# Kernel tuning notes

Hardware: AMD Instinct MI355X
Metric: run time of the kernel (lower is better)

The kernel has to match this reference:

```python
import jax, jax.numpy as jnp
import numpy as np

N_USER = 250_000
N_ITEM = 250_000
E = 500_000
IN, H, C = 128, 64, 2
NEG_SLOPE = 0.01  # torch F.leaky_relu default


def setup_inputs() -> dict:
    key = jax.random.key(0)
    ks = jax.random.split(key, 24)
    d = {}
    d["feat_user"] = jax.random.normal(ks[0], (N_USER, IN), jnp.float32)
    d["feat_item"] = jax.random.normal(ks[1], (N_ITEM, IN), jnp.float32)
    # per-etype linear params, layer 1 (in_feats -> h_dim)
    s1 = 1.0 / np.sqrt(IN)
    d["W1_follows"] = jax.random.normal(ks[2], (IN, H), jnp.float32) * s1
    d["b1_follows"] = jax.random.normal(ks[3], (H,), jnp.float32) * s1
    d["W1_clicks"]  = jax.random.normal(ks[4], (IN, H), jnp.float32) * s1
    d["b1_clicks"]  = jax.random.normal(ks[5], (H,), jnp.float32) * s1
    d["W1_rev"]     = jax.random.normal(ks[6], (IN, H), jnp.float32) * s1
    d["b1_rev"]     = jax.random.normal(ks[7], (H,), jnp.float32) * s1
    # per-etype linear params, layer 2 (h_dim -> num_classes)
    s2 = 1.0 / np.sqrt(H)
    d["W2_follows"] = jax.random.normal(ks[8], (H, C), jnp.float32) * s2
    d["b2_follows"] = jax.random.normal(ks[9], (C,), jnp.float32) * s2
    d["W2_clicks"]  = jax.random.normal(ks[10], (H, C), jnp.float32) * s2
    d["b2_clicks"]  = jax.random.normal(ks[11], (C,), jnp.float32) * s2
    d["W2_rev"]     = jax.random.normal(ks[12], (H, C), jnp.float32) * s2
    d["b2_rev"]     = jax.random.normal(ks[13], (C,), jnp.float32) * s2
    # edge lists: (src, dst) per canonical etype
    d["follows_src"] = jax.random.randint(ks[14], (E,), 0, N_USER, jnp.int32)  # user->user
    d["follows_dst"] = jax.random.randint(ks[15], (E,), 0, N_USER, jnp.int32)
    d["clicks_src"]  = jax.random.randint(ks[16], (E,), 0, N_USER, jnp.int32)  # user->item
    d["clicks_dst"]  = jax.random.randint(ks[17], (E,), 0, N_ITEM, jnp.int32)
    d["rev_src"]     = jax.random.randint(ks[18], (E,), 0, N_ITEM, jnp.int32)  # item->user
    d["rev_dst"]     = jax.random.randint(ks[19], (E,), 0, N_USER, jnp.int32)
    return d


def _mean_agg(Wh, src, dst, n_dst):
    # copy_u + mean: gather transformed src feats per edge, segment-mean onto dst
    m = Wh[src]                                                   # [E, d]
    s = jax.ops.segment_sum(m, dst, num_segments=n_dst)           # [n_dst, d]
    deg = jax.ops.segment_sum(jnp.ones_like(dst, Wh.dtype), dst, num_segments=n_dst)
    return s / jnp.maximum(deg, 1.0)[:, None]                     # 0 for deg-0 nodes (DGL fills 0)


def _layer(fu, fi, Wf, bf, Wc, bc, Wr, br,
           fsrc, fdst, csrc, cdst, rsrc, rdst):
    # per-etype linear on src features, per-etype mean, cross-etype 'sum'
    h_user = (_mean_agg(fu @ Wf + bf, fsrc, fdst, N_USER)
              + _mean_agg(fi @ Wr + br, rsrc, rdst, N_USER))
    h_item = _mean_agg(fu @ Wc + bc, csrc, cdst, N_ITEM)
    return h_user, h_item


def reference(feat_user, feat_item,
              W1_follows, b1_follows, W1_clicks, b1_clicks, W1_rev, b1_rev,
              W2_follows, b2_follows, W2_clicks, b2_clicks, W2_rev, b2_rev,
              follows_src, follows_dst, clicks_src, clicks_dst, rev_src, rev_dst):
    h1u, h1i = _layer(feat_user, feat_item,
                      W1_follows, b1_follows, W1_clicks, b1_clicks, W1_rev, b1_rev,
                      follows_src, follows_dst, clicks_src, clicks_dst, rev_src, rev_dst)
    h2u = jnp.where(h1u >= 0, h1u, NEG_SLOPE * h1u)
    h2i = jnp.where(h1i >= 0, h1i, NEG_SLOPE * h1i)
    out_u, out_i = _layer(h2u, h2i,
                          W2_follows, b2_follows, W2_clicks, b2_clicks, W2_rev, b2_rev,
                          follows_src, follows_dst, clicks_src, clicks_dst, rev_src, rev_dst)
    # (h_dict, h_dict_2) flattened per ntype
    return (out_u, out_i, h2u, h2i)
```

## Files before the change

### kernel.cpp

```cpp
#include <hip/hip_runtime.h>
#include <cstdio>

#define NU 250000
#define NI 250000
#define NE 500000
#define ND 250000
#define NB_SCAN 245
#define NR 8
#define RSZ 31250

typedef __attribute__((ext_vector_type(8))) short short8v;
typedef __attribute__((ext_vector_type(4))) float float4v;

__device__ inline unsigned short f2bf(float x) {
  unsigned int b = __float_as_uint(x);
  unsigned int r = (b + 0x7FFFu + ((b >> 16) & 1u)) >> 16;
  return (unsigned short)r;
}
__device__ inline float bf2f(unsigned short u) {
  return __uint_as_float(((unsigned int)u) << 16);
}

__device__ inline void async_copy16(const float* g, float* l) {
  __builtin_amdgcn_global_load_lds((const __attribute__((address_space(1))) void*)g,
                                   (__attribute__((address_space(3))) void*)l, 16, 0, 0);
}

__global__ void hist3_kernel(const int* __restrict__ fdst, const int* __restrict__ cdst,
                             const int* __restrict__ rdst,
                             int* __restrict__ degf, int* __restrict__ degc, int* __restrict__ degr) {
  int i = blockIdx.x * blockDim.x + threadIdx.x;
  if (i < NE) {
    atomicAdd(&degf[fdst[i]], 1);
    atomicAdd(&degc[cdst[i]], 1);
    atomicAdd(&degr[rdst[i]], 1);
  }
}

__global__ void scan1_kernel(const int* __restrict__ deg0, const int* __restrict__ deg1,
                             const int* __restrict__ deg2, int* __restrict__ bsum) {
  const int* deg = blockIdx.y == 0 ? deg0 : (blockIdx.y == 1 ? deg1 : deg2);
  int* bs = bsum + blockIdx.y * 256;
  __shared__ int s[256];
  int b = blockIdx.x, t = threadIdx.x;
  int base = b * 1024 + t * 4;
  int v = 0;
  #pragma unroll
  for (int i = 0; i < 4; ++i) if (base + i < ND) v += deg[base + i];
  s[t] = v; __syncthreads();
  for (int off = 128; off > 0; off >>= 1) { if (t < off) s[t] += s[t + off]; __syncthreads(); }
  if (t == 0) bs[b] = s[0];
}

__global__ void scan2_kernel(int* __restrict__ bsum) {
  int* bs = bsum + blockIdx.x * 256;
  __shared__ int s[256];
  int t = threadIdx.x;
  s[t] = (t < NB_SCAN) ? bs[t] : 0;
  __syncthreads();
  for (int off = 1; off < 256; off <<= 1) {
    int x = (t >= off) ? s[t - off] : 0;
    __syncthreads();
    s[t] += x;
    __syncthreads();
  }
  if (t < NB_SCAN) bs[t] = (t == 0) ? 0 : s[t - 1];
}

__global__ void scan3_kernel(const int* __restrict__ deg0, const int* __restrict__ deg1,
                             const int* __restrict__ deg2, const int* __restrict__ bsum,
                             int* __restrict__ offs0, int* __restrict__ offs1, int* __restrict__ offs2,
                             int* __restrict__ cur0, int* __restrict__ cur1, int* __restrict__ cur2) {
  int y = blockIdx.y;
  const int* deg = y == 0 ? deg0 : (y == 1 ? deg1 : deg2);
  int* offs = y == 0 ? offs0 : (y == 1 ? offs1 : offs2);
  int* cursor = y == 0 ? cur0 : (y == 1 ? cur1 : cur2);
  const int* bs = bsum + y * 256;
  __shared__ int s[256];
  int b = blockIdx.x, t = threadIdx.x;
  int base = b * 1024 + t * 4;
  int v[4]; int sum = 0;
  #pragma unroll
  for (int i = 0; i < 4; ++i) { v[i] = (base + i < ND) ? deg[base + i] : 0; sum += v[i]; }
  s[t] = sum; __syncthreads();
  for (int off = 1; off < 256; off <<= 1) {
    int x = (t >= off) ? s[t - off] : 0;
    __syncthreads();
    s[t] += x;
    __syncthreads();
  }
  int run = bs[b] + s[t] - sum;
  #pragma unroll
  for (int i = 0; i < 4; ++i) {
    if (base + i < ND) { offs[base + i] = run; cursor[base + i] = run; run += v[i]; }
  }
  if (b == 0 && t == 0) offs[ND] = NE;
}

__global__ void bucket_part_kernel(const int* __restrict__ fsrc, const int* __restrict__ fdst,
                                   const int* __restrict__ csrc, const int* __restrict__ cdst,
                                   const int* __restrict__ rsrc, const int* __restrict__ rdst,
                                   int* __restrict__ curf, int* __restrict__ curc, int* __restrict__ curr,
                                   int* __restrict__ srtf, int* __restrict__ srtc, int* __restrict__ srtr) {
  const int r = blockIdx.x & (NR - 1);
  const int chunk = blockIdx.x >> 3;
  const int lo = r * RSZ, hi = lo + RSZ;
  const int base = chunk * 1024;
  #pragma unroll
  for (int i = 0; i < 4; ++i) {
    int e = base + i * 256 + threadIdx.x;
    if (e < NE) {
      int d0 = fdst[e]; int s0 = fsrc[e];
      if (d0 >= lo && d0 < hi) { int p = atomicAdd(&curf[d0], 1); srtf[p] = s0; }
      int d1 = cdst[e]; int s1 = csrc[e];
      if (d1 >= lo && d1 < hi) { int p = atomicAdd(&curc[d1], 1); srtc[p] = s1; }
      int d2 = rdst[e]; int s2 = rsrc[e];
      if (d2 >= lo && d2 < hi) { int p = atomicAdd(&curr[d2], 1); srtr[p] = s2; }
    }
  }
}

__global__ void prepw_kernel(const float* __restrict__ W0, const float* __restrict__ W1,
                             const float* __restrict__ W2, unsigned short* __restrict__ T) {
  int gt = blockIdx.x * 256 + threadIdx.x;
  int et = gt >> 10;
  int g = gt & 1023;
  int gl = g & 63;
  int jm = (g >> 6) & 3;
  int c = g >> 8;
  int kb = c * 32 + (gl >> 4) * 8;
  int col = jm * 16 + (gl & 15);
  const float* W = et == 0 ? W0 : (et == 1 ? W1 : W2);
  short8v u;
  #pragma unroll
  for (int i = 0; i < 8; ++i) u[i] = (short)f2bf(W[(kb + i) * 64 + col]);
  ((short8v*)T)[gt] = u;
}

template <bool TWO>
__global__ __launch_bounds__(256, 2) void gemm_dma_kernel(
    const float* __restrict__ X, int n, int ntiles,
    const unsigned short* __restrict__ Ta, const float* __restrict__ ba,
    const unsigned short* __restrict__ Tb, const float* __restrict__ bb,
    unsigned short* __restrict__ Ya, unsigned short* __restrict__ Yb) {
  __shared__ float sx[2][64 * 128];
  const int tid = threadIdx.x;
  const int lane = tid & 63;
  const int wave = tid >> 6;
  const int cb = (lane >> 4) * 4;

  short8v A[4][4], B[4][4];
  #pragma unroll
  for (int c = 0; c < 4; ++c) {
    #pragma unroll
    for (int jm = 0; jm < 4; ++jm) {
      A[c][jm] = ((const short8v*)Ta)[c * 256 + jm * 64 + lane];
      if constexpr (TWO) B[c][jm] = ((const short8v*)Tb)[c * 256 + jm * 64 + lane];
    }
  }
  float4 bias_a[4], bias_b[4];
  #pragma unroll
  for (int jm = 0; jm < 4; ++jm) {
    bias_a[jm] = *(const float4*)&ba[jm * 16 + cb];
    if constexpr (TWO) bias_b[jm] = *(const float4*)&bb[jm * 16 + cb];
  }

  const int nl = wave * 16 + (lane & 15);
  const int sw = nl & 7;

  int t = blockIdx.x;
  {
    #pragma unroll
    for (int j = 0; j < 8; ++j) {
      int idx = (wave * 8 + j) * 64 + lane;
      int row = idx >> 5, u = idx & 31;
      int gr = t * 64 + row; if (gr >= n) gr = n - 1;
      const float* src = X + (size_t)gr * 128 + ((u ^ (row & 7)) << 2);
      float* dst = &sx[0][(wave * 8 + j) * 256];
      async_copy16(src, dst);
    }
  }
  asm volatile("s_waitcnt vmcnt(0)" ::: "memory");
  __syncthreads();

  int cur = 0;
  while (true) {
    int tn = t + (int)gridDim.x;
    bool more = (tn < ntiles);
    if (more) {
      #pragma unroll
      for (int j = 0; j < 8; ++j) {
        int idx = (wave * 8 + j) * 64 + lane;
        int row = idx >> 5, u = idx & 31;
        int gr = tn * 64 + row; if (gr >= n) gr = n - 1;
        const float* src = X + (size_t)gr * 128 + ((u ^ (row & 7)) << 2);
        float* dst = &sx[cur ^ 1][(wave * 8 + j) * 256];
        async_copy16(src, dst);
      }
    }

    float4v accA[4] = {};
    float4v accB[4] = {};
    #pragma unroll
    for (int c = 0; c < 4; ++c) {
      int s0 = c * 8 + (lane >> 4) * 2;
      float4 f0 = *(const float4*)&sx[cur][nl * 128 + (((s0 + 0) ^ sw) << 2)];
      float4 f1 = *(const float4*)&sx[cur][nl * 128 + (((s0 + 1) ^ sw) << 2)];
      short8v bfr;
      bfr[0] = (short)f2bf(f0.x); bfr[1] = (short)f2bf(f0.y);
      bfr[2] = (short)f2bf(f0.z); bfr[3] = (short)f2bf(f0.w);
      bfr[4] = (short)f2bf(f1.x); bfr[5] = (short)f2bf(f1.y);
      bfr[6] = (short)f2bf(f1.z); bfr[7] = (short)f2bf(f1.w);
      #pragma unroll
      for (int jm = 0; jm < 4; ++jm) {
        accA[jm] = __builtin_amdgcn_mfma_f32_16x16x32_bf16(A[c][jm], bfr, accA[jm], 0, 0, 0);
        if constexpr (TWO)
          accB[jm] = __builtin_amdgcn_mfma_f32_16x16x32_bf16(B[c][jm], bfr, accB[jm], 0, 0, 0);
      }
    }
    int node = t * 64 + nl;
    if (node < n) {
      #pragma unroll
      for (int jm = 0; jm < 4; ++jm) {
        ushort4 o;
        o.x = f2bf(accA[jm][0] + bias_a[jm].x);
        o.y = f2bf(accA[jm][1] + bias_a[jm].y);
        o.z = f2bf(accA[jm][2] + bias_a[jm].z);
        o.w = f2bf(accA[jm][3] + bias_a[jm].w);
        *(ushort4*)&Ya[(size_t)node * 64 + jm * 16 + cb] = o;
        if constexpr (TWO) {
          ushort4 o2;
          o2.x = f2bf(accB[jm][0] + bias_b[jm].x);
          o2.y = f2bf(accB[jm][1] + bias_b[jm].y);
          o2.z = f2bf(accB[jm][2] + bias_b[jm].z);
          o2.w = f2bf(accB[jm][3] + bias_b[jm].w);
          *(ushort4*)&Yb[(size_t)node * 64 + jm * 16 + cb] = o2;
        }
      }
    }

    if (!more) break;
    asm volatile("s_waitcnt vmcnt(0)" ::: "memory");
    __syncthreads();
    cur ^= 1;
    t = tn;
  }
}

__global__ __launch_bounds__(256) void agg_user_kernel(
    const unsigned short* __restrict__ Whf, const unsigned short* __restrict__ Whr,
    const int* __restrict__ offs_f, const int* __restrict__ srt_f,
    const int* __restrict__ offs_r, const int* __restrict__ srt_r,
    const float* __restrict__ W2f, const float* __restrict__ b2f,
    const float* __restrict__ W2c, const float* __restrict__ b2c,
    float* __restrict__ h2u, float* __restrict__ Y2f, float* __restrict__ Y2c) {
  int t = blockIdx.x * 256 + threadIdx.x;
  int d = t >> 4, q = t & 15;
  if (d >= NU) return;

  float af[4] = {0.f, 0.f, 0.f, 0.f};
  int f0 = offs_f[d], f1 = offs_f[d + 1];
  for (int e = f0; e < f1; ++e) {
    int s = srt_f[e];
    ushort4 v = *(const ushort4*)&Whf[(size_t)s * 64 + q * 4];
    af[0] += bf2f(v.x); af[1] += bf2f(v.y); af[2] += bf2f(v.z); af[3] += bf2f(v.w);
  }
  float rf = 1.0f / fmaxf((float)(f1 - f0), 1.0f);

  float ar[4] = {0.f, 0.f, 0.f, 0.f};
  int r0 = offs_r[d], r1 = offs_r[d + 1];
  for (int e = r0; e < r1; ++e) {
    int s = srt_r[e];
    ushort4 v = *(const ushort4*)&Whr[(size_t)s * 64 + q * 4];
    ar[0] += bf2f(v.x); ar[1] += bf2f(v.y); ar[2] += bf2f(v.z); ar[3] += bf2f(v.w);
  }
  float rr = 1.0f / fmaxf((float)(r1 - r0), 1.0f);

  float h[4];
  #pragma unroll
  for (int i = 0; i < 4; ++i) {
    float x = af[i] * rf + ar[i] * rr;
    h[i] = x >= 0.f ? x : 0.01f * x;
  }
  *(float4*)&h2u[(size_t)d * 64 + q * 4] = make_float4(h[0], h[1], h[2], h[3]);

  float pf0 = 0.f, pf1 = 0.f, pc0 = 0.f, pc1 = 0.f;
  #pragma unroll
  for (int i = 0; i < 4; ++i) {
    int j = q * 4 + i;
    pf0 += h[i] * W2f[j * 2 + 0]; pf1 += h[i] * W2f[j * 2 + 1];
    pc0 += h[i] * W2c[j * 2 + 0]; pc1 += h[i] * W2c[j * 2 + 1];
  }
  #pragma unroll
  for (int off = 1; off < 16; off <<= 1) {
    pf0 += __shfl_xor(pf0, off, 64);
    pf1 += __shfl_xor(pf1, off, 64);
    pc0 += __shfl_xor(pc0, off, 64);
    pc1 += __shfl_xor(pc1, off, 64);
  }
  if (q == 0) {
    Y2f[(size_t)d * 2 + 0] = pf0 + b2f[0];
    Y2f[(size_t)d * 2 + 1] = pf1 + b2f[1];
    Y2c[(size_t)d * 2 + 0] = pc0 + b2c[0];
    Y2c[(size_t)d * 2 + 1] = pc1 + b2c[1];
  }
}

__global__ __launch_bounds__(256) void agg_item_kernel(
    const unsigned short* __restrict__ Whc,
    const int* __restrict__ offs_c, const int* __restrict__ srt_c,
    const float* __restrict__ W2r, const float* __restrict__ b2r,
    float* __restrict__ h2i, float* __restrict__ Y2r) {
  int t = blockIdx.x * 256 + threadIdx.x;
  int d = t >> 4, q = t & 15;
  if (d >= NI) return;

  float ac[4] = {0.f, 0.f, 0.f, 0.f};
  int c0 = offs_c[d], c1 = offs_c[d + 1];
  for (int e = c0; e < c1; ++e) {
    int s = srt_c[e];
    ushort4 v = *(const ushort4*)&Whc[(size_t)s * 64 + q * 4];
    ac[0] += bf2f(v.x); ac[1] += bf2f(v.y); ac[2] += bf2f(v.z); ac[3] += bf2f(v.w);
  }
  float rc = 1.0f / fmaxf((float)(c1 - c0), 1.0f);

  float h[4];
  #pragma unroll
  for (int i = 0; i < 4; ++i) {
    float x = ac[i] * rc;
    h[i] = x >= 0.f ? x : 0.01f * x;
  }
  *(float4*)&h2i[(size_t)d * 64 + q * 4] = make_float4(h[0], h[1], h[2], h[3]);

  float p0 = 0.f, p1 = 0.f;
  #pragma unroll
  for (int i = 0; i < 4; ++i) {
    int j = q * 4 + i;
    p0 += h[i] * W2r[j * 2 + 0]; p1 += h[i] * W2r[j * 2 + 1];
  }
  #pragma unroll
  for (int off = 1; off < 16; off <<= 1) {
    p0 += __shfl_xor(p0, off, 64);
    p1 += __shfl_xor(p1, off, 64);
  }
  if (q == 0) {
    Y2r[(size_t)d * 2 + 0] = p0 + b2r[0];
    Y2r[(size_t)d * 2 + 1] = p1 + b2r[1];
  }
}

__global__ void out_user_kernel(const float* __restrict__ Y2f, const float* __restrict__ Y2r,
                                const int* __restrict__ offs_f, const int* __restrict__ srt_f,
                                const int* __restrict__ offs_r, const int* __restrict__ srt_r,
                                float* __restrict__ out_u) {
  int d = blockIdx.x * blockDim.x + threadIdx.x;
  if (d >= NU) return;
  int f0 = offs_f[d], f1 = offs_f[d + 1];
  float a0 = 0.f, a1 = 0.f;
  for (int e = f0; e < f1; ++e) {
    int s = srt_f[e];
    a0 += Y2f[(size_t)s * 2 + 0]; a1 += Y2f[(size_t)s * 2 + 1];
  }
  float rf = 1.0f / fmaxf((float)(f1 - f0), 1.0f);
  int r0 = offs_r[d], r1 = offs_r[d + 1];
  float c0 = 0.f, c1 = 0.f;
  for (int e = r0; e < r1; ++e) {
    int s = srt_r[e];
    c0 += Y2r[(size_t)s * 2 + 0]; c1 += Y2r[(size_t)s * 2 + 1];
  }
  float rr = 1.0f / fmaxf((float)(r1 - r0), 1.0f);
  out_u[(size_t)d * 2 + 0] = a0 * rf + c0 * rr;
  out_u[(size_t)d * 2 + 1] = a1 * rf + c1 * rr;
}

__global__ void out_item_kernel(const float* __restrict__ Y2c,
                                const int* __restrict__ offs_c, const int* __restrict__ srt_c,
                                float* __restrict__ out_i) {
  int d = blockIdx.x * blockDim.x + threadIdx.x;
  if (d >= NI) return;
  int c0o = offs_c[d], c1o = offs_c[d + 1];
  float a0 = 0.f, a1 = 0.f;
  for (int e = c0o; e < c1o; ++e) {
    int s = srt_c[e];
    a0 += Y2c[(size_t)s * 2 + 0]; a1 += Y2c[(size_t)s * 2 + 1];
  }
  float rc = 1.0f / fmaxf((float)(c1o - c0o), 1.0f);
  out_i[(size_t)d * 2 + 0] = a0 * rc;
  out_i[(size_t)d * 2 + 1] = a1 * rc;
}

extern "C" void kernel_launch(void* const* d_in, const int* in_sizes, int n_in,
                              void* d_out, int out_size, void* d_ws, size_t ws_size,
                              hipStream_t stream) {
  const float* feat_user = (const float*)d_in[0];
  const float* feat_item = (const float*)d_in[1];
  const float* W1f = (const float*)d_in[2];  const float* b1f = (const float*)d_in[3];
  const float* W1c = (const float*)d_in[4];  const float* b1c = (const float*)d_in[5];
  const float* W1r = (const float*)d_in[6];  const float* b1r = (const float*)d_in[7];
  const float* W2f = (const float*)d_in[8];  const float* b2f = (const float*)d_in[9];
  const float* W2c = (const float*)d_in[10]; const float* b2c = (const float*)d_in[11];
  const float* W2r = (const float*)d_in[12]; const float* b2r = (const float*)d_in[13];
  const int* fsrc = (const int*)d_in[14];  const int* fdst = (const int*)d_in[15];
  const int* csrc = (const int*)d_in[16];  const int* cdst = (const int*)d_in[17];
  const int* rsrc = (const int*)d_in[18];  const int* rdst = (const int*)d_in[19];

  float* out = (float*)d_out;
  float* out_u = out;
  float* out_i = out + 2 * NU;
  float* h2u  = out + 1000000;
  float* h2i  = out + 17000000;

  unsigned short* Whf = (unsigned short*)d_ws;
  unsigned short* Whc = Whf + 16000000;
  unsigned short* Whr = Whc + 16000000;
  unsigned short* Wtab = Whr + 16000000;
  unsigned short* Tf = Wtab;
  unsigned short* Tc = Wtab + 8192;
  unsigned short* Tr = Wtab + 16384;
  int* ibase = (int*)(Wtab + 24576);
  const int P = 250304;
  int* offs_f = ibase;            int* offs_c = offs_f + P;  int* offs_r = offs_c + P;
  int* cur_f  = offs_r + P;       int* cur_c  = cur_f + P;   int* cur_r  = cur_c + P;
  int* deg_f  = cur_r + P;        int* deg_c  = deg_f + P;   int* deg_r  = deg_c + P;
  int* srt_f  = deg_r + P;
  int* srt_c  = srt_f + 500096;
  int* srt_r  = srt_c + 500096;
  int* bsum   = srt_r + 500096;
  float* Y2f  = (float*)(bsum + 768);
  float* Y2c  = Y2f + 500000;
  float* Y2r  = Y2c + 500000;

  size_t need = 96000000ull + 24576ull * 2ull
              + (9ull * P + 3ull * 500096ull + 768ull + 1500000ull) * 4ull;
  if (ws_size < need) {
    fprintf(stderr, "kernel_launch: ws too small (%zu < %zu)\n", ws_size, need);
    return;
  }

  hipMemsetAsync(deg_f, 0, (size_t)(3 * P) * 4, stream);

  const int eb = (NE + 255) / 256;

  prepw_kernel<<<12, 256, 0, stream>>>(W1f, W1c, W1r, Wtab);

  const int utiles = (NU + 63) / 64;
  const int itiles = (NI + 63) / 64;
  gemm_dma_kernel<true><<<512, 256, 0, stream>>>(feat_user, NU, utiles, Tf, b1f, Tc, b1c, Whf, Whc);
  gemm_dma_kernel<false><<<512, 256, 0, stream>>>(feat_item, NI, itiles, Tr, b1r, nullptr, nullptr, Whr, nullptr);

  hist3_kernel<<<eb, 256, 0, stream>>>(fdst, cdst, rdst, deg_f, deg_c, deg_r);
  scan1_kernel<<<dim3(NB_SCAN, 3), 256, 0, stream>>>(deg_f, deg_c, deg_r, bsum);
  scan2_kernel<<<3, 256, 0, stream>>>(bsum);
  scan3_kernel<<<dim3(NB_SCAN, 3), 256, 0, stream>>>(deg_f, deg_c, deg_r, bsum,
                                                     offs_f, offs_c, offs_r,
                                                     cur_f, cur_c, cur_r);
  const int chunks = (NE + 1023) / 1024;
  bucket_part_kernel<<<chunks * NR, 256, 0, stream>>>(fsrc, fdst, csrc, cdst, rsrc, rdst,
                                                      cur_f, cur_c, cur_r, srt_f, srt_c, srt_r);

  const int ab = (NU * 16 + 255) / 256;
  agg_user_kernel<<<ab, 256, 0, stream>>>(Whf, Whr, offs_f, srt_f, offs_r, srt_r,
                                          W2f, b2f, W2c, b2c, h2u, Y2f, Y2c);
  agg_item_kernel<<<ab, 256, 0, stream>>>(Whc, offs_c, srt_c, W2r, b2r, h2i, Y2r);

  const int nb = (NU + 255) / 256;
  out_user_kernel<<<nb, 256, 0, stream>>>(Y2f, Y2r, offs_f, srt_f, offs_r, srt_r, out_u);
  out_item_kernel<<<nb, 256, 0, stream>>>(Y2c, offs_c, srt_c, out_i);
}
```

Before: 353.6 us.

## Fuse user/item aggregation kernels and interleave gathers for memory-level parallelism

Merges the user and item aggregation kernels into one launch, and the two output kernels into another, using a block-index split. Each 16-lane group now handles two destination nodes, and the follows and rev edge lists are walked together in one loop, so several independent gathers are in flight per iteration. The aim is more overlap of gather latency and fewer launches. In exchange the code is more divergent and uses more registers, and there are fewer threads per node.

```diff
diff --git a/kernel.cpp b/kernel.cpp
--- a/kernel.cpp
+++ b/kernel.cpp
@@ -247,146 +247,177 @@
   }
 }
 
-__global__ __launch_bounds__(256) void agg_user_kernel(
+__global__ __launch_bounds__(256) void agg_fused_kernel(
     const unsigned short* __restrict__ Whf, const unsigned short* __restrict__ Whr,
+    const unsigned short* __restrict__ Whc,
     const int* __restrict__ offs_f, const int* __restrict__ srt_f,
     const int* __restrict__ offs_r, const int* __restrict__ srt_r,
+    const int* __restrict__ offs_c, const int* __restrict__ srt_c,
     const float* __restrict__ W2f, const float* __restrict__ b2f,
     const float* __restrict__ W2c, const float* __restrict__ b2c,
-    float* __restrict__ h2u, float* __restrict__ Y2f, float* __restrict__ Y2c) {
-  int t = blockIdx.x * 256 + threadIdx.x;
-  int d = t >> 4, q = t & 15;
-  if (d >= NU) return;
-
-  float af[4] = {0.f, 0.f, 0.f, 0.f};
-  int f0 = offs_f[d], f1 = offs_f[d + 1];
-  for (int e = f0; e < f1; ++e) {
-    int s = srt_f[e];
-    ushort4 v = *(const ushort4*)&Whf[(size_t)s * 64 + q * 4];
-    af[0] += bf2f(v.x); af[1] += bf2f(v.y); af[2] += bf2f(v.z); af[3] += bf2f(v.w);
-  }
-  float rf = 1.0f / fmaxf((float)(f1 - f0), 1.0f);
-
-  float ar[4] = {0.f, 0.f, 0.f, 0.f};
-  int r0 = offs_r[d], r1 = offs_r[d + 1];
-  for (int e = r0; e < r1; ++e) {
-    int s = srt_r[e];
-    ushort4 v = *(const ushort4*)&Whr[(size_t)s * 64 + q * 4];
-    ar[0] += bf2f(v.x); ar[1] += bf2f(v.y); ar[2] += bf2f(v.z); ar[3] += bf2f(v.w);
-  }
-  float rr = 1.0f / fmaxf((float)(r1 - r0), 1.0f);
-
-  float h[4];
-  #pragma unroll
-  for (int i = 0; i < 4; ++i) {
-    float x = af[i] * rf + ar[i] * rr;
-    h[i] = x >= 0.f ? x : 0.01f * x;
-  }
-  *(float4*)&h2u[(size_t)d * 64 + q * 4] = make_float4(h[0], h[1], h[2], h[3]);
-
-  float pf0 = 0.f, pf1 = 0.f, pc0 = 0.f, pc1 = 0.f;
-  #pragma unroll
-  for (int i = 0; i < 4; ++i) {
-    int j = q * 4 + i;
-    pf0 += h[i] * W2f[j * 2 + 0]; pf1 += h[i] * W2f[j * 2 + 1];
-    pc0 += h[i] * W2c[j * 2 + 0]; pc1 += h[i] * W2c[j * 2 + 1];
-  }
-  #pragma unroll
-  for (int off = 1; off < 16; off <<= 1) {
-    pf0 += __shfl_xor(pf0, off, 64);
-    pf1 += __shfl_xor(pf1, off, 64);
-    pc0 += __shfl_xor(pc0, off, 64);
-    pc1 += __shfl_xor(pc1, off, 64);
-  }
-  if (q == 0) {
-    Y2f[(size_t)d * 2 + 0] = pf0 + b2f[0];
-    Y2f[(size_t)d * 2 + 1] = pf1 + b2f[1];
-    Y2c[(size_t)d * 2 + 0] = pc0 + b2c[0];
-    Y2c[(size_t)d * 2 + 1] = pc1 + b2c[1];
-  }
-}
-
-__global__ __launch_bounds__(256) void agg_item_kernel(
-    const unsigned short* __restrict__ Whc,
-    const int* __restrict__ offs_c, const int* __restrict__ srt_c,
     const float* __restrict__ W2r, const float* __restrict__ b2r,
-    float* __restrict__ h2i, float* __restrict__ Y2r) {
-  int t = blockIdx.x * 256 + threadIdx.x;
-  int d = t >> 4, q = t & 15;
-  if (d >= NI) return;
-
-  float ac[4] = {0.f, 0.f, 0.f, 0.f};
-  int c0 = offs_c[d], c1 = offs_c[d + 1];
-  for (int e = c0; e < c1; ++e) {
-    int s = srt_c[e];
-    ushort4 v = *(const ushort4*)&Whc[(size_t)s * 64 + q * 4];
-    ac[0] += bf2f(v.x); ac[1] += bf2f(v.y); ac[2] += bf2f(v.z); ac[3] += bf2f(v.w);
-  }
-  float rc = 1.0f / fmaxf((float)(c1 - c0), 1.0f);
-
-  float h[4];
-  #pragma unroll
-  for (int i = 0; i < 4; ++i) {
-    float x = ac[i] * rc;
-    h[i] = x >= 0.f ? x : 0.01f * x;
-  }
-  *(float4*)&h2i[(size_t)d * 64 + q * 4] = make_float4(h[0], h[1], h[2], h[3]);
-
-  float p0 = 0.f, p1 = 0.f;
-  #pragma unroll
-  for (int i = 0; i < 4; ++i) {
-    int j = q * 4 + i;
-    p0 += h[i] * W2r[j * 2 + 0]; p1 += h[i] * W2r[j * 2 + 1];
-  }
-  #pragma unroll
-  for (int off = 1; off < 16; off <<= 1) {
-    p0 += __shfl_xor(p0, off, 64);
-    p1 += __shfl_xor(p1, off, 64);
-  }
-  if (q == 0) {
-    Y2r[(size_t)d * 2 + 0] = p0 + b2r[0];
-    Y2r[(size_t)d * 2 + 1] = p1 + b2r[1];
-  }
-}
-
-__global__ void out_user_kernel(const float* __restrict__ Y2f, const float* __restrict__ Y2r,
-                                const int* __restrict__ offs_f, const int* __restrict__ srt_f,
-                                const int* __restrict__ offs_r, const int* __restrict__ srt_r,
-                                float* __restrict__ out_u) {
-  int d = blockIdx.x * blockDim.x + threadIdx.x;
-  if (d >= NU) return;
-  int f0 = offs_f[d], f1 = offs_f[d + 1];
-  float a0 = 0.f, a1 = 0.f;
-  for (int e = f0; e < f1; ++e) {
-    int s = srt_f[e];
-    a0 += Y2f[(size_t)s * 2 + 0]; a1 += Y2f[(size_t)s * 2 + 1];
-  }
-  float rf = 1.0f / fmaxf((float)(f1 - f0), 1.0f);
-  int r0 = offs_r[d], r1 = offs_r[d + 1];
-  float c0 = 0.f, c1 = 0.f;
-  for (int e = r0; e < r1; ++e) {
-    int s = srt_r[e];
-    c0 += Y2r[(size_t)s * 2 + 0]; c1 += Y2r[(size_t)s * 2 + 1];
-  }
-  float rr = 1.0f / fmaxf((float)(r1 - r0), 1.0f);
-  out_u[(size_t)d * 2 + 0] = a0 * rf + c0 * rr;
-  out_u[(size_t)d * 2 + 1] = a1 * rf + c1 * rr;
-}
-
-__global__ void out_item_kernel(const float* __restrict__ Y2c,
-                                const int* __restrict__ offs_c, const int* __restrict__ srt_c,
-                                float* __restrict__ out_i) {
-  int d = blockIdx.x * blockDim.x + threadIdx.x;
-  if (d >= NI) return;
-  int c0o = offs_c[d], c1o = offs_c[d + 1];
-  float a0 = 0.f, a1 = 0.f;
-  for (int e = c0o; e < c1o; ++e) {
-    int s = srt_c[e];
-    a0 += Y2c[(size_t)s * 2 + 0]; a1 += Y2c[(size_t)s * 2 + 1];
-  }
-  float rc = 1.0f / fmaxf((float)(c1o - c0o), 1.0f);
-  out_i[(size_t)d * 2 + 0] = a0 * rc;
-  out_i[(size_t)d * 2 + 1] = a1 * rc;
+    float* __restrict__ h2u, float* __restrict__ h2i,
+    float* __restrict__ Y2f, float* __restrict__ Y2c, float* __restrict__ Y2r,
+    int ub) {
+  const int tid = threadIdx.x;
+  const int gid = tid >> 4;
+  const int q = tid & 15;
+
+  if (blockIdx.x < ub) {
+    int d0 = (blockIdx.x * 16 + gid) * 2;
+    int d1 = d0 + 1;
+    bool v0 = d0 < NU, v1 = d1 < NU;
+    int ef0 = v0 ? offs_f[d0] : 0, ef0e = v0 ? offs_f[d0 + 1] : 0;
+    int ef1 = v1 ? offs_f[d1] : 0, ef1e = v1 ? offs_f[d1 + 1] : 0;
+    int er0 = v0 ? offs_r[d0] : 0, er0e = v0 ? offs_r[d0 + 1] : 0;
+    int er1 = v1 ? offs_r[d1] : 0, er1e = v1 ? offs_r[d1 + 1] : 0;
+    float rf0 = 1.0f / fmaxf((float)(ef0e - ef0), 1.0f);
+    float rf1 = 1.0f / fmaxf((float)(ef1e - ef1), 1.0f);
+    float rr0 = 1.0f / fmaxf((float)(er0e - er0), 1.0f);
+    float rr1 = 1.0f / fmaxf((float)(er1e - er1), 1.0f);
+
+    float af0[4] = {0, 0, 0, 0}, af1[4] = {0, 0, 0, 0};
+    float ar0[4] = {0, 0, 0, 0}, ar1[4] = {0, 0, 0, 0};
+    while (ef0 < ef0e || ef1 < ef1e || er0 < er0e || er1 < er1e) {
+      bool hf0 = ef0 < ef0e, hf1 = ef1 < ef1e, hr0 = er0 < er0e, hr1 = er1 < er1e;
+      ushort4 vf0, vf1, vr0, vr1;
+      if (hf0) { int s = srt_f[ef0]; vf0 = *(const ushort4*)&Whf[(size_t)s * 64 + q * 4]; }
+      if (hf1) { int s = srt_f[ef1]; vf1 = *(const ushort4*)&Whf[(size_t)s * 64 + q * 4]; }
+      if (hr0) { int s = srt_r[er0]; vr0 = *(const ushort4*)&Whr[(size_t)s * 64 + q * 4]; }
+      if (hr1) { int s = srt_r[er1]; vr1 = *(const ushort4*)&Whr[(size_t)s * 64 + q * 4]; }
+      if (hf0) { af0[0] += bf2f(vf0.x); af0[1] += bf2f(vf0.y); af0[2] += bf2f(vf0.z); af0[3] += bf2f(vf0.w); ++ef0; }
+      if (hf1) { af1[0] += bf2f(vf1.x); af1[1] += bf2f(vf1.y); af1[2] += bf2f(vf1.z); af1[3] += bf2f(vf1.w); ++ef1; }
+      if (hr0) { ar0[0] += bf2f(vr0.x); ar0[1] += bf2f(vr0.y); ar0[2] += bf2f(vr0.z); ar0[3] += bf2f(vr0.w); ++er0; }
+      if (hr1) { ar1[0] += bf2f(vr1.x); ar1[1] += bf2f(vr1.y); ar1[2] += bf2f(vr1.z); ar1[3] += bf2f(vr1.w); ++er1; }
+    }
+
+    float h0v[4], h1v[4];
+    #pragma unroll
+    for (int i = 0; i < 4; ++i) {
+      float x0 = af0[i] * rf0 + ar0[i] * rr0;
+      h0v[i] = x0 >= 0.f ? x0 : 0.01f * x0;
+      float x1 = af1[i] * rf1 + ar1[i] * rr1;
+      h1v[i] = x1 >= 0.f ? x1 : 0.01f * x1;
+    }
+    if (v0) *(float4*)&h2u[(size_t)d0 * 64 + q * 4] = make_float4(h0v[0], h0v[1], h0v[2], h0v[3]);
+    if (v1) *(float4*)&h2u[(size_t)d1 * 64 + q * 4] = make_float4(h1v[0], h1v[1], h1v[2], h1v[3]);
+
+    float pf00 = 0, pf01 = 0, pc00 = 0, pc01 = 0;
+    float pf10 = 0, pf11 = 0, pc10 = 0, pc11 = 0;
+    #pragma unroll
+    for (int i = 0; i < 4; ++i) {
+      int j = q * 4 + i;
+      float wf0 = W2f[j * 2 + 0], wf1 = W2f[j * 2 + 1];
+      float wc0 = W2c[j * 2 + 0], wc1 = W2c[j * 2 + 1];
+      pf00 += h0v[i] * wf0; pf01 += h0v[i] * wf1;
+      pc00 += h0v[i] * wc0; pc01 += h0v[i] * wc1;
+      pf10 += h1v[i] * wf0; pf11 += h1v[i] * wf1;
+      pc10 += h1v[i] * wc0; pc11 += h1v[i] * wc1;
+    }
+    #pragma unroll
+    for (int off = 1; off < 16; off <<= 1) {
+      pf00 += __shfl_xor(pf00, off, 64); pf01 += __shfl_xor(pf01, off, 64);
+      pc00 += __shfl_xor(pc00, off, 64); pc01 += __shfl_xor(pc01, off, 64);
+      pf10 += __shfl_xor(pf10, off, 64); pf11 += __shfl_xor(pf11, off, 64);
+      pc10 += __shfl_xor(pc10, off, 64); pc11 += __shfl_xor(pc11, off, 64);
+    }
+    if (q == 0) {
+      if (v0) {
+        Y2f[(size_t)d0 * 2 + 0] = pf00 + b2f[0]; Y2f[(size_t)d0 * 2 + 1] = pf01 + b2f[1];
+        Y2c[(size_t)d0 * 2 + 0] = pc00 + b2c[0]; Y2c[(size_t)d0 * 2 + 1] = pc01 + b2c[1];
+      }
+      if (v1) {
+        Y2f[(size_t)d1 * 2 + 0] = pf10 + b2f[0]; Y2f[(size_t)d1 * 2 + 1] = pf11 + b2f[1];
+        Y2c[(size_t)d1 * 2 + 0] = pc10 + b2c[0]; Y2c[(size_t)d1 * 2 + 1] = pc11 + b2c[1];
+      }
+    }
+  } else {
+    int d0 = ((blockIdx.x - ub) * 16 + gid) * 2;
+    int d1 = d0 + 1;
+    bool v0 = d0 < NI, v1 = d1 < NI;
+    int ec0 = v0 ? offs_c[d0] : 0, ec0e = v0 ? offs_c[d0 + 1] : 0;
+    int ec1 = v1 ? offs_c[d1] : 0, ec1e = v1 ? offs_c[d1 + 1] : 0;
+    float rc0 = 1.0f / fmaxf((float)(ec0e - ec0), 1.0f);
+    float rc1 = 1.0f / fmaxf((float)(ec1e - ec1), 1.0f);
+
+    float ac0[4] = {0, 0, 0, 0}, ac1[4] = {0, 0, 0, 0};
+    while (ec0 < ec0e || ec1 < ec1e) {
+      bool h0 = ec0 < ec0e, h1 = ec1 < ec1e;
+      ushort4 v0v, v1v;
+      if (h0) { int s = srt_c[ec0]; v0v = *(const ushort4*)&Whc[(size_t)s * 64 + q * 4]; }
+      if (h1) { int s = srt_c[ec1]; v1v = *(const ushort4*)&Whc[(size_t)s * 64 + q * 4]; }
+      if (h0) { ac0[0] += bf2f(v0v.x); ac0[1] += bf2f(v0v.y); ac0[2] += bf2f(v0v.z); ac0[3] += bf2f(v0v.w); ++ec0; }
+      if (h1) { ac1[0] += bf2f(v1v.x); ac1[1] += bf2f(v1v.y); ac1[2] += bf2f(v1v.z); ac1[3] += bf2f(v1v.w); ++ec1; }
+    }
+
+    float h0v[4], h1v[4];
+    #pragma unroll
+    for (int i = 0; i < 4; ++i) {
+      float x0 = ac0[i] * rc0;
+      h0v[i] = x0 >= 0.f ? x0 : 0.01f * x0;
+      float x1 = ac1[i] * rc1;
+      h1v[i] = x1 >= 0.f ? x1 : 0.01f * x1;
+    }
+    if (v0) *(float4*)&h2i[(size_t)d0 * 64 + q * 4] = make_float4(h0v[0], h0v[1], h0v[2], h0v[3]);
+    if (v1) *(float4*)&h2i[(size_t)d1 * 64 + q * 4] = make_float4(h1v[0], h1v[1], h1v[2], h1v[3]);
+
+    float p00 = 0, p01 = 0, p10 = 0, p11 = 0;
+    #pragma unroll
+    for (int i = 0; i < 4; ++i) {
+      int j = q * 4 + i;
+      float w0 = W2r[j * 2 + 0], w1 = W2r[j * 2 + 1];
+      p00 += h0v[i] * w0; p01 += h0v[i] * w1;
+      p10 += h1v[i] * w0; p11 += h1v[i] * w1;
+    }
+    #pragma unroll
+    for (int off = 1; off < 16; off <<= 1) {
+      p00 += __shfl_xor(p00, off, 64); p01 += __shfl_xor(p01, off, 64);
+      p10 += __shfl_xor(p10, off, 64); p11 += __shfl_xor(p11, off, 64);
+    }
+    if (q == 0) {
+      if (v0) { Y2r[(size_t)d0 * 2 + 0] = p00 + b2r[0]; Y2r[(size_t)d0 * 2 + 1] = p01 + b2r[1]; }
+      if (v1) { Y2r[(size_t)d1 * 2 + 0] = p10 + b2r[0]; Y2r[(size_t)d1 * 2 + 1] = p11 + b2r[1]; }
+    }
+  }
+}
+
+__global__ void out_fused_kernel(const float* __restrict__ Y2f, const float* __restrict__ Y2r,
+                                 const float* __restrict__ Y2c,
+                                 const int* __restrict__ offs_f, const int* __restrict__ srt_f,
+                                 const int* __restrict__ offs_r, const int* __restrict__ srt_r,
+                                 const int* __restrict__ offs_c, const int* __restrict__ srt_c,
+                                 float* __restrict__ out_u, float* __restrict__ out_i, int ub) {
+  if (blockIdx.x < ub) {
+    int d = blockIdx.x * 256 + threadIdx.x;
+    if (d >= NU) return;
+    int f = offs_f[d], f1 = offs_f[d + 1];
+    int r = offs_r[d], r1 = offs_r[d + 1];
+    float rf = 1.0f / fmaxf((float)(f1 - f), 1.0f);
+    float rr = 1.0f / fmaxf((float)(r1 - r), 1.0f);
+    float a0 = 0.f, a1 = 0.f, c0 = 0.f, c1 = 0.f;
+    while (f < f1 || r < r1) {
+      bool hf = f < f1, hr = r < r1;
+      float2 yf, yr;
+      if (hf) { int s = srt_f[f]; yf = *(const float2*)&Y2f[(size_t)s * 2]; }
+      if (hr) { int s = srt_r[r]; yr = *(const float2*)&Y2r[(size_t)s * 2]; }
+      if (hf) { a0 += yf.x; a1 += yf.y; ++f; }
+      if (hr) { c0 += yr.x; c1 += yr.y; ++r; }
+    }
+    out_u[(size_t)d * 2 + 0] = a0 * rf + c0 * rr;
+    out_u[(size_t)d * 2 + 1] = a1 * rf + c1 * rr;
+  } else {
+    int d = (blockIdx.x - ub) * 256 + threadIdx.x;
+    if (d >= NI) return;
+    int c = offs_c[d], c1e = offs_c[d + 1];
+    float rc = 1.0f / fmaxf((float)(c1e - c), 1.0f);
+    float a0 = 0.f, a1 = 0.f;
+    for (; c < c1e; ++c) {
+      int s = srt_c[c];
+      a0 += Y2c[(size_t)s * 2 + 0]; a1 += Y2c[(size_t)s * 2 + 1];
+    }
+    out_i[(size_t)d * 2 + 0] = a0 * rc;
+    out_i[(size_t)d * 2 + 1] = a1 * rc;
+  }
 }
 
 extern "C" void kernel_launch(void* const* d_in, const int* in_sizes, int n_in,
@@ -458,12 +489,14 @@
   bucket_part_kernel<<<chunks * NR, 256, 0, stream>>>(fsrc, fdst, csrc, cdst, rsrc, rdst,
                                                       cur_f, cur_c, cur_r, srt_f, srt_c, srt_r);
 
-  const int ab = (NU * 16 + 255) / 256;
-  agg_user_kernel<<<ab, 256, 0, stream>>>(Whf, Whr, offs_f, srt_f, offs_r, srt_r,
-                                          W2f, b2f, W2c, b2c, h2u, Y2f, Y2c);
-  agg_item_kernel<<<ab, 256, 0, stream>>>(Whc, offs_c, srt_c, W2r, b2r, h2i, Y2r);
-
-  const int nb = (NU + 255) / 256;
-  out_user_kernel<<<nb, 256, 0, stream>>>(Y2f, Y2r, offs_f, srt_f, offs_r, srt_r, out_u);
-  out_item_kernel<<<nb, 256, 0, stream>>>(Y2c, offs_c, srt_c, out_i);
-}
+  const int ub = (NU + 31) / 32;
+  agg_fused_kernel<<<2 * ub, 256, 0, stream>>>(Whf, Whr, Whc,
+                                               offs_f, srt_f, offs_r, srt_r, offs_c, srt_c,
+                                               W2f, b2f, W2c, b2c, W2r, b2r,
+                                               h2u, h2i, Y2f, Y2c, Y2r, ub);
+
+  const int ob = (NU + 255) / 256;
+  out_fused_kernel<<<2 * ob, 256, 0, stream>>>(Y2f, Y2r, Y2c,
+                                               offs_f, srt_f, offs_r, srt_r, offs_c, srt_c,
+                                               out_u, out_i, ob);
+}
```

Result: faster. 344.7 us (-2.5%).
